# Performance work log

Hardware: AMD Instinct MI355X
Metric: run time of the kernel (lower is better)

Reference implementation:

```python
import jax, jax.numpy as jnp
import numpy as np

CHANNELS = 256
CODEBOOK_SIZE = 8192
UPDATE_SPEED = 0.01
N_TOKENS = 32768


def setup_inputs() -> dict:
    key = jax.random.key(0)
    k1, k2 = jax.random.split(key)
    embeddings = jax.random.normal(k1, (N_TOKENS, CHANNELS), dtype=jnp.float32)
    code_usage = jnp.ones((CODEBOOK_SIZE,), dtype=jnp.float32)
    code_embedding_sum = jax.random.normal(k2, (CODEBOOK_SIZE, CHANNELS), dtype=jnp.float32)
    return {"embeddings": embeddings, "code_usage": code_usage,
            "code_embedding_sum": code_embedding_sum}


def reference(embeddings, code_usage, code_embedding_sum):
    # codebook from EMA statistics: [K, C]
    codebook = code_embedding_sum / jnp.clip(code_usage, 1e-5, None)[:, None]

    # encode: nearest code by Euclidean distance. argmin over codes is
    # invariant under sqrt, so use squared distances (avoids sqrt of [K, N]).
    cb_sq = jnp.sum(codebook * codebook, axis=-1)            # [K]
    x_sq = jnp.sum(embeddings * embeddings, axis=-1)         # [N]
    # d2[k, n] = ||cb_k - x_n||^2
    d2 = cb_sq[:, None] - 2.0 * jnp.einsum('kc,nc->kn', codebook, embeddings) + x_sq[None, :]
    codes = jnp.argmin(d2, axis=0).astype(jnp.int32)         # [N]

    # decode: gather codebook rows
    quantized = jnp.take(codebook, codes, axis=0)            # [N, C]

    # straight-through estimator
    embeddings_q = embeddings + jax.lax.stop_gradient(quantized - embeddings)

    # commitment loss: mse(stop_grad(embeddings_q), embeddings)
    diff = jax.lax.stop_gradient(embeddings_q) - embeddings
    commitment_loss = jnp.mean(diff * diff)

    # EMA updates (training mode, under no_grad in the original)
    n = embeddings.shape[0]
    counts = jax.ops.segment_sum(jnp.ones((n,), dtype=code_usage.dtype),
                                 codes, num_segments=CODEBOOK_SIZE)
    emb_sum = jax.ops.segment_sum(embeddings, codes, num_segments=CODEBOOK_SIZE)
    s = jnp.float32(UPDATE_SPEED)
    new_code_usage = jax.lax.stop_gradient(code_usage * (1.0 - s) + counts * s)
    new_code_embedding_sum = jax.lax.stop_gradient(
        code_embedding_sum * (1.0 - s) + emb_sum * s)

    return codes, embeddings_q, commitment_loss, new_code_usage, new_code_embedding_sum
```

## Files before the change

kernel.cpp:

```cpp
#include <hip/hip_runtime.h>

#define CH 256
#define KC 8192
#define KCP 8448
#define NT 32768

#define TM 128
#define TN 128
#define BK 32
#define YS 3
#define JQ (KCP / YS)
#define NSTG ((JQ / TN) * (CH / BK))

typedef _Float16 half4_t __attribute__((ext_vector_type(4)));
typedef _Float16 half8_t __attribute__((ext_vector_type(8)));
typedef float floatx4 __attribute__((ext_vector_type(4)));

typedef __attribute__((address_space(1))) const unsigned int guint_t;
typedef __attribute__((address_space(3))) unsigned int luint_t;

__device__ __forceinline__ int swz(int row, int chunk) {
    return row * BK + ((chunk ^ ((row >> 1) & 3)) << 3);
}

__global__ void k_prep(const float* __restrict__ usage,
                       const float* __restrict__ ces,
                       const float* __restrict__ emb,
                       _Float16* __restrict__ cbh,
                       _Float16* __restrict__ cbl,
                       float* __restrict__ cbsq,
                       _Float16* __restrict__ eh,
                       _Float16* __restrict__ el,
                       int* __restrict__ hist,
                       unsigned long long* __restrict__ packed) {
    int b = blockIdx.x, t = threadIdx.x;
    if (b < KCP) {
        if (b < KC) {
            float uc = fmaxf(usage[b], 1e-5f);
            float v  = ces[b * CH + t];
            float cb = v / uc;
            _Float16 h = (_Float16)cb;
            cbh[b * CH + t] = h;
            cbl[b * CH + t] = (_Float16)(cb - (float)h);

            float p = cb * cb;
            #pragma unroll
            for (int off = 32; off; off >>= 1) p += __shfl_down(p, off);
            __shared__ float ps[4];
            int lane = t & 63, w = t >> 6;
            if (lane == 0) ps[w] = p;
            __syncthreads();
            if (t == 0) cbsq[b] = ps[0] + ps[1] + ps[2] + ps[3];
            if (t == 1) hist[b] = 0;
            int gid = b * CH + t;
            if (gid < NT) packed[gid] = 0xFFFFFFFFFFFFFFFFull;
        } else {
            cbh[b * CH + t] = (_Float16)0.0f;
            cbl[b * CH + t] = (_Float16)0.0f;
            if (t == 0) cbsq[b] = 3.0e38f;
        }
    } else {
        int i = (b - KCP) * 256 + t;
        float4 v = ((const float4*)emb)[i];
        float va[4] = {v.x, v.y, v.z, v.w};
        half4_t h, l;
        #pragma unroll
        for (int q = 0; q < 4; ++q) {
            _Float16 hh = (_Float16)va[q];
            h[q] = hh;
            l[q] = (_Float16)(va[q] - (float)hh);
        }
        ((half4_t*)eh)[i] = h;
        ((half4_t*)el)[i] = l;
    }
}

__launch_bounds__(256, 2)
__global__ void k_argmin(const _Float16* __restrict__ eh,
                         const _Float16* __restrict__ el,
                         const _Float16* __restrict__ cbh,
                         const _Float16* __restrict__ cbl,
                         const float* __restrict__ cbsq,
                         unsigned long long* __restrict__ packed) {
    __shared__ __align__(16) _Float16 sm[2][4][TM * BK];
    __shared__ float cand_v[2][TM];
    __shared__ int   cand_i[2][TM];

    const int t    = threadIdx.x;
    const int lane = t & 63;
    const int wave = t >> 6;
    const int wx   = wave & 1;
    const int wy   = wave >> 1;
    const int lr   = lane & 15;
    const int koq  = lane >> 4;

    const int n0 = blockIdx.x * TM;
    const int jq = blockIdx.y * JQ;

    const _Float16* dsrc = (wave == 0) ? eh : (wave == 1) ? el
                         : (wave == 2) ? cbh : cbl;
    const int qsw   = (lane & 3) ^ ((lane >> 3) & 3);
    const int lrow  = lane >> 2;

    float minv[16];
    int   mini[16];
    #pragma unroll
    for (int e = 0; e < 16; ++e) { minv[e] = 3.402823466e38f; mini[e] = 0; }

    floatx4 acc[4][4];
    #pragma unroll
    for (int mf = 0; mf < 4; ++mf)
        #pragma unroll
        for (int nf = 0; nf < 4; ++nf)
            acc[mf][nf] = (floatx4){0.f, 0.f, 0.f, 0.f};

    auto dma = [&](int buf, int sg) {
        const int c0 = (sg & 7) * BK;
        const int jb = jq + (sg >> 3) * TN;
        const int rb = (wave < 2) ? n0 : jb;
        const _Float16* gbase = dsrc + (size_t)(rb + lrow) * CH + c0 + qsw * 8;
        #pragma unroll
        for (int i = 0; i < 8; ++i) {
            const _Float16* g = gbase + (size_t)(i * 16) * CH;
            __builtin_amdgcn_global_load_lds(
                (guint_t*)g, (luint_t*)&sm[buf][wave][i * 512], 16, 0, 0);
        }
    };

    dma(0, 0);

    #pragma unroll 1
    for (int s = 0; s < NSTG; ++s) {
        const int cur = s & 1;

        if (s + 1 < NSTG) {
            dma(cur ^ 1, s + 1);
            asm volatile("s_waitcnt vmcnt(8)" ::: "memory");
        } else {
            asm volatile("s_waitcnt vmcnt(0)" ::: "memory");
        }
        __builtin_amdgcn_s_barrier();
        __builtin_amdgcn_sched_barrier(0);

        half8_t fah[4], fal[4];
        #pragma unroll
        for (int mf = 0; mf < 4; ++mf) {
            int off = swz(wy * 64 + mf * 16 + lr, koq);
            fah[mf] = *(const half8_t*)&sm[cur][0][off];
            fal[mf] = *(const half8_t*)&sm[cur][1][off];
        }
        __builtin_amdgcn_s_setprio(1);
        #pragma unroll
        for (int nf = 0; nf < 4; ++nf) {
            int offb = swz(wx * 64 + nf * 16 + lr, koq);
            half8_t fbh = *(const half8_t*)&sm[cur][2][offb];
            half8_t fbl = *(const half8_t*)&sm[cur][3][offb];
            #pragma unroll
            for (int mf = 0; mf < 4; ++mf) {
                acc[mf][nf] = __builtin_amdgcn_mfma_f32_16x16x32_f16(
                    fah[mf], fbh, acc[mf][nf], 0, 0, 0);
                acc[mf][nf] = __builtin_amdgcn_mfma_f32_16x16x32_f16(
                    fah[mf], fbl, acc[mf][nf], 0, 0, 0);
                acc[mf][nf] = __builtin_amdgcn_mfma_f32_16x16x32_f16(
                    fal[mf], fbh, acc[mf][nf], 0, 0, 0);
            }
        }
        __builtin_amdgcn_s_setprio(0);

        if ((s & 7) == 7) {
            int jbase = jq + (s >> 3) * TN;
            #pragma unroll
            for (int nf = 0; nf < 4; ++nf) {
                int j = jbase + wx * 64 + nf * 16 + lr;
                float sq = cbsq[j];
                #pragma unroll
                for (int mf = 0; mf < 4; ++mf) {
                    floatx4 a = acc[mf][nf];
                    #pragma unroll
                    for (int r = 0; r < 4; ++r) {
                        float sc = sq - 2.0f * a[r];
                        int e = mf * 4 + r;
                        if (sc < minv[e]) { minv[e] = sc; mini[e] = j; }
                    }
                    acc[mf][nf] = (floatx4){0.f, 0.f, 0.f, 0.f};
                }
            }
        }

        asm volatile("s_waitcnt lgkmcnt(0)" ::: "memory");
        __builtin_amdgcn_sched_barrier(0);
        __builtin_amdgcn_s_barrier();
    }

    #pragma unroll
    for (int e = 0; e < 16; ++e) {
        float v = minv[e];
        int   x = mini[e];
        #pragma unroll
        for (int m = 1; m <= 8; m <<= 1) {
            float ov = __shfl_xor(v, m, 64);
            int   ox = __shfl_xor(x, m, 64);
            if (ov < v || (ov == v && ox < x)) { v = ov; x = ox; }
        }
        if (lr == 0) {
            int row = wy * 64 + (e >> 2) * 16 + (lane >> 4) * 4 + (e & 3);
            cand_v[wx][row] = v;
            cand_i[wx][row] = x;
        }
    }
    __syncthreads();

    if (t < TM) {
        float v0 = cand_v[0][t]; int i0 = cand_i[0][t];
        float v1 = cand_v[1][t]; int i1 = cand_i[1][t];
        if (v1 < v0 || (v1 == v0 && i1 < i0)) { v0 = v1; i0 = i1; }
        unsigned sb = __float_as_uint(v0);
        sb = (sb & 0x80000000u) ? ~sb : (sb | 0x80000000u);
        unsigned long long key = ((unsigned long long)sb << 32) | (unsigned)i0;
        atomicMin(&packed[n0 + t], key);
    }
}

__global__ void k_gather(const float* __restrict__ emb,
                         const float* __restrict__ ces,
                         const float* __restrict__ usage,
                         const unsigned long long* __restrict__ packed,
                         float* __restrict__ out_eq,
                         float* __restrict__ codes_f,
                         int* __restrict__ hist,
                         float* __restrict__ partials) {
    int t = threadIdx.x;
    int wave = t >> 6, lane = t & 63;
    int n = blockIdx.x * 4 + wave;
    int k = (int)(packed[n] & 0xFFFFFFFFull);
    float uc = fmaxf(usage[k], 1e-5f);
    int c = lane * 4;

    float4 e = *(const float4*)&emb[(size_t)n * CH + c];
    float4 v = *(const float4*)&ces[(size_t)k * CH + c];
    float ea[4] = {e.x, e.y, e.z, e.w};
    float va[4] = {v.x, v.y, v.z, v.w};
    float eqa[4];
    float p = 0.0f;
    #pragma unroll
    for (int q = 0; q < 4; ++q) {
        float cb = va[q] / uc;
        float eq = ea[q] + (cb - ea[q]);
        eqa[q] = eq;
        float d = eq - ea[q];
        p += d * d;
    }
    *(float4*)&out_eq[(size_t)n * CH + c] =
        (float4){eqa[0], eqa[1], eqa[2], eqa[3]};

    #pragma unroll
    for (int off = 32; off; off >>= 1) p += __shfl_down(p, off);
    __shared__ float ps[4];
    if (lane == 0) {
        ps[wave] = p;
        codes_f[n] = (float)k;
        atomicAdd(&hist[k], 1);
    }
    __syncthreads();
    if (t == 0) partials[blockIdx.x] = ps[0] + ps[1] + ps[2] + ps[3];
}

__global__ void k_scan(const int* __restrict__ hist,
                       int* __restrict__ offs,
                       int* __restrict__ cursor) {
    __shared__ int bs[256];
    int t = threadIdx.x;
    int base = t * 32;
    int loc[32];
    int s = 0;
    #pragma unroll
    for (int i = 0; i < 32; ++i) { loc[i] = s; s += hist[base + i]; }
    int mysum = s;
    bs[t] = s;
    __syncthreads();
    for (int off = 1; off < 256; off <<= 1) {
        int v = (t >= off) ? bs[t - off] : 0;
        __syncthreads();
        bs[t] += v;
        __syncthreads();
    }
    int excl = bs[t] - mysum;
    #pragma unroll
    for (int i = 0; i < 32; ++i) {
        int o = excl + loc[i];
        offs[base + i]   = o;
        cursor[base + i] = o;
    }
}

__global__ void k_scatter(const unsigned long long* __restrict__ packed,
                          int* __restrict__ cursor,
                          int* __restrict__ bucket) {
    int n = blockIdx.x * 256 + threadIdx.x;
    int k = (int)(packed[n] & 0xFFFFFFFFull);
    int pos = atomicAdd(&cursor[k], 1);
    bucket[pos] = n;
}

__global__ void k_ema(const float* __restrict__ emb,
                      const float* __restrict__ ces,
                      const float* __restrict__ usage,
                      const int* __restrict__ hist,
                      const int* __restrict__ offs,
                      const int* __restrict__ bucket,
                      float* __restrict__ out_ces,
                      float* __restrict__ out_usage) {
    const float s = 0.01f;
    const float oms = 1.0f - s;
    int k = blockIdx.x, t = threadIdx.x;
    int start = offs[k], cnt = hist[k];
    float sum = 0.0f;
    #pragma unroll 2
    for (int i = 0; i < cnt; ++i) {
        int n = bucket[start + i];
        sum += emb[(size_t)n * CH + t];
    }
    out_ces[(size_t)k * CH + t] = oms * ces[(size_t)k * CH + t] + s * sum;
    if (t == 0) out_usage[k] = oms * usage[k] + s * (float)cnt;
}

__global__ void k_final(const float* __restrict__ partials,
                        float* __restrict__ out_loss) {
    int t = threadIdx.x;
    float p = 0.0f;
    for (int i = t; i < NT / 4; i += 256) p += partials[i];
    #pragma unroll
    for (int off = 32; off; off >>= 1) p += __shfl_down(p, off);
    __shared__ float ps[4];
    if ((t & 63) == 0) ps[t >> 6] = p;
    __syncthreads();
    if (t == 0)
        out_loss[0] = (ps[0] + ps[1] + ps[2] + ps[3]) * (1.0f / 8388608.0f);
}

extern "C" void kernel_launch(void* const* d_in, const int* in_sizes, int n_in,
                              void* d_out, int out_size, void* d_ws, size_t ws_size,
                              hipStream_t stream) {
    const float* emb   = (const float*)d_in[0];
    const float* usage = (const float*)d_in[1];
    const float* ces   = (const float*)d_in[2];

    float* out      = (float*)d_out;
    float* o_codes  = out;
    float* o_eq     = out + NT;
    float* o_loss   = o_eq + (size_t)NT * CH;
    float* o_usage  = o_loss + 1;
    float* o_ces    = o_usage + KC;

    unsigned long long* packed = (unsigned long long*)d_ws;
    float* cbsq     = (float*)(packed + NT);
    float* partials = cbsq + KCP;
    int* hist   = (int*)(partials + NT / 4);
    int* offs   = hist + KC;
    int* cursor = offs + KC;
    int* bucket = cursor + KC;
    _Float16* eh  = (_Float16*)(bucket + NT);
    _Float16* el  = eh + (size_t)NT * CH;
    _Float16* cbh = el + (size_t)NT * CH;
    _Float16* cbl = cbh + (size_t)KCP * CH;

    k_prep<<<KCP + NT * CH / 1024, 256, 0, stream>>>(
        usage, ces, emb, cbh, cbl, cbsq, eh, el, hist, packed);
    dim3 agrid(NT / TM, YS);
    k_argmin<<<agrid, 256, 0, stream>>>(eh, el, cbh, cbl, cbsq, packed);
    k_gather<<<NT / 4, 256, 0, stream>>>(emb, ces, usage, packed, o_eq,
                                         o_codes, hist, partials);
    k_scan<<<1, 256, 0, stream>>>(hist, offs, cursor);
    k_scatter<<<NT / 256, 256, 0, stream>>>(packed, cursor, bucket);
    k_ema<<<KC, 256, 0, stream>>>(emb, ces, usage, hist, offs, bucket,
                                  o_ces, o_usage);
    k_final<<<1, 256, 0, stream>>>(partials, o_loss);
}
```

Baseline: 706.9 us.

## Remap argmin grid for XCD locality and restructure the double-buffered DMA pipeline

The argmin grid is changed from a 3-way codebook split over a padded 8448-code range to a 2-way split over the exact 8192 codes. This drops the padding rows and the sentinel fill in the prep kernel. Blocks are launched on a 1-D grid and remapped so consecutive block IDs on the same XCD share token tiles and codebook halves, aiming for better L2 reuse. The stage loop now issues the next-stage DMA without waiting first and does a single full vmcnt wait plus barrier at the end of each stage. Codebook squared norms are prefetched into registers at the start of each tile. This trades some prefetch depth (a full drain each stage) for fewer sync points, and changes the occupancy balance with 512 blocks instead of 768.

```diff
diff --git a/kernel.cpp b/kernel.cpp
--- a/kernel.cpp
+++ b/kernel.cpp
@@ -2,14 +2,13 @@
 
 #define CH 256
 #define KC 8192
-#define KCP 8448
 #define NT 32768
 
 #define TM 128
 #define TN 128
 #define BK 32
-#define YS 3
-#define JQ (KCP / YS)
+#define YS 2
+#define JQ (KC / YS)
 #define NSTG ((JQ / TN) * (CH / BK))
 
 typedef _Float16 half4_t __attribute__((ext_vector_type(4)));
@@ -34,33 +33,27 @@
                        int* __restrict__ hist,
                        unsigned long long* __restrict__ packed) {
     int b = blockIdx.x, t = threadIdx.x;
-    if (b < KCP) {
-        if (b < KC) {
-            float uc = fmaxf(usage[b], 1e-5f);
-            float v  = ces[b * CH + t];
-            float cb = v / uc;
-            _Float16 h = (_Float16)cb;
-            cbh[b * CH + t] = h;
-            cbl[b * CH + t] = (_Float16)(cb - (float)h);
-
-            float p = cb * cb;
-            #pragma unroll
-            for (int off = 32; off; off >>= 1) p += __shfl_down(p, off);
-            __shared__ float ps[4];
-            int lane = t & 63, w = t >> 6;
-            if (lane == 0) ps[w] = p;
-            __syncthreads();
-            if (t == 0) cbsq[b] = ps[0] + ps[1] + ps[2] + ps[3];
-            if (t == 1) hist[b] = 0;
-            int gid = b * CH + t;
-            if (gid < NT) packed[gid] = 0xFFFFFFFFFFFFFFFFull;
-        } else {
-            cbh[b * CH + t] = (_Float16)0.0f;
-            cbl[b * CH + t] = (_Float16)0.0f;
-            if (t == 0) cbsq[b] = 3.0e38f;
-        }
+    if (b < KC) {
+        float uc = fmaxf(usage[b], 1e-5f);
+        float v  = ces[b * CH + t];
+        float cb = v / uc;
+        _Float16 h = (_Float16)cb;
+        cbh[b * CH + t] = h;
+        cbl[b * CH + t] = (_Float16)(cb - (float)h);
+
+        float p = cb * cb;
+        #pragma unroll
+        for (int off = 32; off; off >>= 1) p += __shfl_down(p, off);
+        __shared__ float ps[4];
+        int lane = t & 63, w = t >> 6;
+        if (lane == 0) ps[w] = p;
+        __syncthreads();
+        if (t == 0) cbsq[b] = ps[0] + ps[1] + ps[2] + ps[3];
+        if (t == 1) hist[b] = 0;
+        int gid = b * CH + t;
+        if (gid < NT) packed[gid] = 0xFFFFFFFFFFFFFFFFull;
     } else {
-        int i = (b - KCP) * 256 + t;
+        int i = (b - KC) * 256 + t;
         float4 v = ((const float4*)emb)[i];
         float va[4] = {v.x, v.y, v.z, v.w};
         half4_t h, l;
@@ -94,8 +87,10 @@
     const int lr   = lane & 15;
     const int koq  = lane >> 4;
 
-    const int n0 = blockIdx.x * TM;
-    const int jq = blockIdx.y * JQ;
+    const int id  = blockIdx.x;
+    const int xcd = id & 7;
+    const int n0  = ((id >> 3) * 4 + (xcd & 3)) * TM;
+    const int jq  = (xcd >> 2) * JQ;
 
     const _Float16* dsrc = (wave == 0) ? eh : (wave == 1) ? el
                          : (wave == 2) ? cbh : cbl;
@@ -128,19 +123,24 @@
     };
 
     dma(0, 0);
+    asm volatile("s_waitcnt vmcnt(0)" ::: "memory");
+    __builtin_amdgcn_s_barrier();
+    __builtin_amdgcn_sched_barrier(0);
+
+    float csq[4] = {0.f, 0.f, 0.f, 0.f};
 
     #pragma unroll 1
     for (int s = 0; s < NSTG; ++s) {
         const int cur = s & 1;
 
-        if (s + 1 < NSTG) {
-            dma(cur ^ 1, s + 1);
-            asm volatile("s_waitcnt vmcnt(8)" ::: "memory");
-        } else {
-            asm volatile("s_waitcnt vmcnt(0)" ::: "memory");
-        }
-        __builtin_amdgcn_s_barrier();
-        __builtin_amdgcn_sched_barrier(0);
+        if ((s & 7) == 0) {
+            int jbase = jq + (s >> 3) * TN;
+            #pragma unroll
+            for (int nf = 0; nf < 4; ++nf)
+                csq[nf] = cbsq[jbase + wx * 64 + nf * 16 + lr];
+        }
+
+        if (s + 1 < NSTG) dma(cur ^ 1, s + 1);
 
         half8_t fah[4], fal[4];
         #pragma unroll
@@ -172,7 +172,7 @@
             #pragma unroll
             for (int nf = 0; nf < 4; ++nf) {
                 int j = jbase + wx * 64 + nf * 16 + lr;
-                float sq = cbsq[j];
+                float sq = csq[nf];
                 #pragma unroll
                 for (int mf = 0; mf < 4; ++mf) {
                     floatx4 a = acc[mf][nf];
@@ -187,9 +187,10 @@
             }
         }
 
-        asm volatile("s_waitcnt lgkmcnt(0)" ::: "memory");
+        asm volatile("s_waitcnt vmcnt(0)" ::: "memory");
         __builtin_amdgcn_sched_barrier(0);
         __builtin_amdgcn_s_barrier();
+        __builtin_amdgcn_sched_barrier(0);
     }
 
     #pragma unroll
@@ -354,7 +355,7 @@
 
     unsigned long long* packed = (unsigned long long*)d_ws;
     float* cbsq     = (float*)(packed + NT);
-    float* partials = cbsq + KCP;
+    float* partials = cbsq + KC;
     int* hist   = (int*)(partials + NT / 4);
     int* offs   = hist + KC;
     int* cursor = offs + KC;
@@ -362,12 +363,12 @@
     _Float16* eh  = (_Float16*)(bucket + NT);
     _Float16* el  = eh + (size_t)NT * CH;
     _Float16* cbh = el + (size_t)NT * CH;
-    _Float16* cbl = cbh + (size_t)KCP * CH;
-
-    k_prep<<<KCP + NT * CH / 1024, 256, 0, stream>>>(
+    _Float16* cbl = cbh + (size_t)KC * CH;
+
+    k_prep<<<KC + NT * CH / 1024, 256, 0, stream>>>(
         usage, ces, emb, cbh, cbl, cbsq, eh, el, hist, packed);
-    dim3 agrid(NT / TM, YS);
-    k_argmin<<<agrid, 256, 0, stream>>>(eh, el, cbh, cbl, cbsq, packed);
+    k_argmin<<<(NT / TM) * YS, 256, 0, stream>>>(eh, el, cbh, cbl, cbsq,
+                                                 packed);
     k_gather<<<NT / 4, 256, 0, stream>>>(emb, ces, usage, packed, o_eq,
                                          o_codes, hist, partials);
     k_scan<<<1, 256, 0, stream>>>(hist, offs, cursor);
```

Result: faster. 675.2 us (-4.5%).
